# Performance work log

Measured on AMD Instinct MI355X. Metric: run time of the kernel, lower is better.

Reference implementation:

```python
import jax, jax.numpy as jnp
import numpy as np

N = 100000
E = 800000
NODE_DIM = 128
EDGE_DIM = 8
NUM_HEADS = 8
HEAD_DIM = NODE_DIM // NUM_HEADS


def setup_inputs() -> dict:
    key = jax.random.key(0)
    k_x, k_ei, k_ea, k_w1, k_b1, k_w2, k_b2 = jax.random.split(key, 7)
    x = jax.random.normal(k_x, (N, NODE_DIM), dtype=jnp.float32)
    edge_index = jax.random.randint(k_ei, (2, E), 0, N, dtype=jnp.int32)
    edge_attr = jax.random.normal(k_ea, (E, EDGE_DIM), dtype=jnp.float32)
    # node_proj: Linear(node_dim, node_dim)
    lim1 = 1.0 / np.sqrt(NODE_DIM)
    W_node = jax.random.uniform(k_w1, (NODE_DIM, NODE_DIM), minval=-lim1, maxval=lim1, dtype=jnp.float32)
    b_node = jax.random.uniform(k_b1, (NODE_DIM,), minval=-lim1, maxval=lim1, dtype=jnp.float32)
    # edge_to_attn: Linear(edge_dim, num_heads) followed by sigmoid
    lim2 = 1.0 / np.sqrt(EDGE_DIM)
    W_edge = jax.random.uniform(k_w2, (NUM_HEADS, EDGE_DIM), minval=-lim2, maxval=lim2, dtype=jnp.float32)
    b_edge = jax.random.uniform(k_b2, (NUM_HEADS,), minval=-lim2, maxval=lim2, dtype=jnp.float32)
    return {"x": x, "edge_index": edge_index, "edge_attr": edge_attr,
            "W_node": W_node, "b_node": b_node, "W_edge": W_edge, "b_edge": b_edge}


def reference(x, edge_index, edge_attr, W_node, b_node, W_edge, b_edge):
    # project node features: [N, node_dim]
    x_proj = x @ W_node.T + b_node
    # per-edge, per-head sigmoid gates: [E, H]
    edge_gates = jax.nn.sigmoid(edge_attr @ W_edge.T + b_edge)
    source = edge_index[0]
    target = edge_index[1]
    # gather source node features: [E, H, head_dim]
    x_source = x_proj[source].reshape(E, NUM_HEADS, HEAD_DIM)
    # gate and flatten messages: [E, node_dim]
    messages = (x_source * edge_gates[:, :, None]).reshape(E, NODE_DIM)
    # scatter-add to target nodes: [N, node_dim]
    out = jax.ops.segment_sum(messages, target, num_segments=N)
    return out
```

## Files before the change

kernel.cpp:

```cpp
#include <hip/hip_runtime.h>

typedef unsigned short u16;
typedef unsigned int u32;
typedef __attribute__((ext_vector_type(8))) short short8;
typedef __attribute__((ext_vector_type(4))) float f32x4;

constexpr int NODES = 100000;
constexpr int EDGES = 800000;
constexpr int DIM = 128;
constexpr int EDIM = 8;
constexpr int HEADS = 8;

__device__ inline u16 f2bf(float f) {
    u32 u = __float_as_uint(f);
    u = (u + 0x7FFFu + ((u >> 16) & 1u)) >> 16;
    return (u16)u;
}
__device__ inline float bf2f(u16 s) {
    return __uint_as_float(((u32)s) << 16);
}
__device__ inline u32 packbf(float a, float b) {
    return (u32)f2bf(a) | ((u32)f2bf(b) << 16);
}

__global__ __launch_bounds__(256) void convert_w(const float* __restrict__ W,
                                                 u16* __restrict__ Wb) {
    int i = blockIdx.x * 256 + threadIdx.x;
    Wb[i] = f2bf(W[i]);
}

__global__ __launch_bounds__(256) void node_proj_mfma(const float* __restrict__ x,
                                                      const u16* __restrict__ Wb,
                                                      const float* __restrict__ bn,
                                                      u16* __restrict__ xpb) {
    __shared__ u16 sW[128 * 136];

    const int tid = threadIdx.x;
    {
        const short8* g = reinterpret_cast<const short8*>(Wb);
        #pragma unroll
        for (int i = tid; i < 128 * 16; i += 256) {
            int row = i >> 4, ch = i & 15;
            *reinterpret_cast<short8*>(&sW[row * 136 + ch * 8]) = g[row * 16 + ch];
        }
    }
    __syncthreads();

    const int w = tid >> 6;
    const int l = tid & 63;
    const int lr = l & 15;
    const int lh = l >> 4;
    const int m0 = blockIdx.x * 128 + w * 32;

    f32x4 acc[2][8];
    #pragma unroll
    for (int mt = 0; mt < 2; ++mt)
        #pragma unroll
        for (int nt = 0; nt < 8; ++nt) acc[mt][nt] = f32x4{0, 0, 0, 0};

    #pragma unroll
    for (int kk = 0; kk < 4; ++kk) {
        const int kb = kk * 32 + lh * 8;
        short8 a0, a1;
        {
            int row = m0 + lr;  row = row < NODES ? row : 0;
            const float* p = x + (size_t)row * DIM + kb;
            float4 f0 = *reinterpret_cast<const float4*>(p);
            float4 f1 = *reinterpret_cast<const float4*>(p + 4);
            a0[0]=f2bf(f0.x); a0[1]=f2bf(f0.y); a0[2]=f2bf(f0.z); a0[3]=f2bf(f0.w);
            a0[4]=f2bf(f1.x); a0[5]=f2bf(f1.y); a0[6]=f2bf(f1.z); a0[7]=f2bf(f1.w);
        }
        {
            int row = m0 + 16 + lr;  row = row < NODES ? row : 0;
            const float* p = x + (size_t)row * DIM + kb;
            float4 f0 = *reinterpret_cast<const float4*>(p);
            float4 f1 = *reinterpret_cast<const float4*>(p + 4);
            a1[0]=f2bf(f0.x); a1[1]=f2bf(f0.y); a1[2]=f2bf(f0.z); a1[3]=f2bf(f0.w);
            a1[4]=f2bf(f1.x); a1[5]=f2bf(f1.y); a1[6]=f2bf(f1.z); a1[7]=f2bf(f1.w);
        }
        #pragma unroll
        for (int nt = 0; nt < 8; ++nt) {
            short8 b = *reinterpret_cast<const short8*>(&sW[(nt * 16 + lr) * 136 + kb]);
            acc[0][nt] = __builtin_amdgcn_mfma_f32_16x16x32_bf16(a0, b, acc[0][nt], 0, 0, 0);
            acc[1][nt] = __builtin_amdgcn_mfma_f32_16x16x32_bf16(a1, b, acc[1][nt], 0, 0, 0);
        }
    }

    float bias[8];
    #pragma unroll
    for (int nt = 0; nt < 8; ++nt) bias[nt] = bn[nt * 16 + lr];

    #pragma unroll
    for (int mt = 0; mt < 2; ++mt) {
        #pragma unroll
        for (int r = 0; r < 4; ++r) {
            int grow = m0 + mt * 16 + lh * 4 + r;
            if (grow < NODES) {
                #pragma unroll
                for (int nt = 0; nt < 8; ++nt)
                    xpb[(size_t)grow * DIM + nt * 16 + lr] =
                        f2bf(acc[mt][nt][r] + bias[nt]);
            }
        }
    }
}

__global__ __launch_bounds__(256) void build_rec(const int* __restrict__ ei,
                                                 const float* __restrict__ ea,
                                                 const float* __restrict__ We,
                                                 const float* __restrict__ be,
                                                 int* __restrict__ head,
                                                 uint4* __restrict__ rec) {
    __shared__ float sW[HEADS * EDIM];
    __shared__ float sb[HEADS];
    if (threadIdx.x < HEADS * EDIM) sW[threadIdx.x] = We[threadIdx.x];
    if (threadIdx.x < HEADS) sb[threadIdx.x] = be[threadIdx.x];
    __syncthreads();

    const int e = blockIdx.x * 256 + threadIdx.x;
    if (e >= EDGES) return;

    const int src = ei[e];
    const int tgt = ei[EDGES + e];
    float4 a0 = *reinterpret_cast<const float4*>(ea + (size_t)e * EDIM);
    float4 a1 = *reinterpret_cast<const float4*>(ea + (size_t)e * EDIM + 4);

    float g[HEADS];
    #pragma unroll
    for (int h = 0; h < HEADS; ++h) {
        const float* w = &sW[h * EDIM];
        float z = sb[h]
                + a0.x * w[0] + a0.y * w[1] + a0.z * w[2] + a0.w * w[3]
                + a1.x * w[4] + a1.y * w[5] + a1.z * w[6] + a1.w * w[7];
        g[h] = 1.0f / (1.0f + __expf(-z));
    }

    int nx = atomicExch(&head[tgt], e);

    uint4 r0, r1;
    r0.x = (u32)nx;
    r0.y = (u32)src;
    r0.z = packbf(g[0], g[1]);
    r0.w = packbf(g[2], g[3]);
    r1.x = packbf(g[4], g[5]);
    r1.y = packbf(g[6], g[7]);
    r1.z = 0; r1.w = 0;
    rec[(size_t)e * 2 + 0] = r0;
    rec[(size_t)e * 2 + 1] = r1;
}

__global__ __launch_bounds__(256) void aggregate_v6(const u16* __restrict__ xpb,
                                                    const int* __restrict__ head,
                                                    const char* __restrict__ recB,
                                                    float* __restrict__ out) {
    const int n = blockIdx.x * 16 + (threadIdx.x >> 4);
    if (n >= NODES) return;
    const int l = threadIdx.x & 15;
    const int h = l >> 1;

    float acc[8];
    #pragma unroll
    for (int i = 0; i < 8; ++i) acc[i] = 0.0f;

    int e = head[n];
    while (e >= 0) {
        const char* r = recB + (size_t)e * 32;
        int2 ns = *reinterpret_cast<const int2*>(r);
        float g = bf2f(*reinterpret_cast<const u16*>(r + 8 + 2 * h));
        short8 u = *reinterpret_cast<const short8*>(
            xpb + (size_t)ns.y * DIM + l * 8);
        #pragma unroll
        for (int i = 0; i < 8; ++i) acc[i] += g * bf2f((u16)u[i]);
        e = ns.x;
    }

    float4 o0 = {acc[0], acc[1], acc[2], acc[3]};
    float4 o1 = {acc[4], acc[5], acc[6], acc[7]};
    float4* op = reinterpret_cast<float4*>(out + (size_t)n * DIM + l * 8);
    op[0] = o0;
    op[1] = o1;
}

__global__ __launch_bounds__(256) void edge_scatter(const int* __restrict__ ei,
                                                    const float* __restrict__ ea,
                                                    const float* __restrict__ We,
                                                    const float* __restrict__ be,
                                                    const u16* __restrict__ xpb,
                                                    float* __restrict__ out) {
    __shared__ float sW[HEADS * EDIM];
    __shared__ float sb[HEADS];
    if (threadIdx.x < HEADS * EDIM) sW[threadIdx.x] = We[threadIdx.x];
    if (threadIdx.x < HEADS) sb[threadIdx.x] = be[threadIdx.x];
    __syncthreads();

    const int t = blockIdx.x * 256 + threadIdx.x;
    const int e = t >> 5;
    const int l = t & 31;
    if (e >= EDGES) return;

    const int src = ei[e];
    const int tgt = ei[EDGES + e];
    const int h = l >> 2;

    float4 ea0 = *reinterpret_cast<const float4*>(ea + (size_t)e * EDIM);
    float4 ea1 = *reinterpret_cast<const float4*>(ea + (size_t)e * EDIM + 4);
    float4 wa = *reinterpret_cast<const float4*>(&sW[h * EDIM]);
    float4 wb = *reinterpret_cast<const float4*>(&sW[h * EDIM + 4]);
    float z = sb[h]
            + ea0.x * wa.x + ea0.y * wa.y + ea0.z * wa.z + ea0.w * wa.w
            + ea1.x * wb.x + ea1.y * wb.y + ea1.z * wb.z + ea1.w * wb.w;
    float g = 1.0f / (1.0f + __expf(-z));

    ushort4 u = *reinterpret_cast<const ushort4*>(xpb + (size_t)src * DIM + l * 4);
    float* op = out + (size_t)tgt * DIM + l * 4;
    unsafeAtomicAdd(op + 0, bf2f(u.x) * g);
    unsafeAtomicAdd(op + 1, bf2f(u.y) * g);
    unsafeAtomicAdd(op + 2, bf2f(u.z) * g);
    unsafeAtomicAdd(op + 3, bf2f(u.w) * g);
}

extern "C" void kernel_launch(void* const* d_in, const int* in_sizes, int n_in,
                              void* d_out, int out_size, void* d_ws, size_t ws_size,
                              hipStream_t stream) {
    const float* x   = (const float*)d_in[0];
    const int*   ei  = (const int*)d_in[1];
    const float* eat = (const float*)d_in[2];
    const float* Wn  = (const float*)d_in[3];
    const float* bn  = (const float*)d_in[4];
    const float* We  = (const float*)d_in[5];
    const float* be  = (const float*)d_in[6];
    float* out = (float*)d_out;

    u16* Wb   = (u16*)d_ws;
    u16* xpb  = Wb + DIM * DIM;
    int* head = (int*)(xpb + (size_t)NODES * DIM);
    char* rec = (char*)(head + NODES);

    const size_t need = (size_t)(DIM * DIM) * 2 + (size_t)NODES * DIM * 2
                      + (size_t)NODES * 4 + (size_t)EDGES * 32;

    convert_w<<<64, 256, 0, stream>>>(Wn, Wb);
    node_proj_mfma<<<(NODES + 127) / 128, 256, 0, stream>>>(x, Wb, bn, xpb);

    if (ws_size >= need) {
        hipMemsetAsync(head, 0xFF, (size_t)NODES * sizeof(int), stream);
        build_rec<<<(EDGES + 255) / 256, 256, 0, stream>>>(ei, eat, We, be,
                                                           head, (uint4*)rec);
        aggregate_v6<<<(NODES + 15) / 16, 256, 0, stream>>>(xpb, head, rec, out);
    } else {
        hipMemsetAsync(d_out, 0, (size_t)out_size * sizeof(float), stream);
        edge_scatter<<<(EDGES * 32) / 256, 256, 0, stream>>>(ei, eat, We, be, xpb, out);
    }
}
```

Before: 121.2 us.

## Fuse projection and edge-record kernels; split adjacency lists into four interleaved chains

Merges weight conversion, node projection and edge-record building into one launch, with blocks split by index range, so the two independent stages can run concurrently and two launches disappear. Each node's linked list becomes four chains selected by edge index mod 4. The aggregation kernel then walks four chains at once, giving more independent memory loads in flight per step. In exchange, each projection block converts the weights to bf16 itself, the head array is four times larger, and lanes do masked extra work when chain lengths differ.

```diff
diff --git a/kernel.cpp b/kernel.cpp
--- a/kernel.cpp
+++ b/kernel.cpp
@@ -11,6 +11,9 @@
 constexpr int EDIM = 8;
 constexpr int HEADS = 8;
 
+constexpr int PROJ_BLOCKS = (NODES + 127) / 128;
+constexpr int REC_BLOCKS  = (EDGES + 255) / 256;
+
 __device__ inline u16 f2bf(float f) {
     u32 u = __float_as_uint(f);
     u = (u + 0x7FFFu + ((u >> 16) & 1u)) >> 16;
@@ -23,134 +26,141 @@
     return (u32)f2bf(a) | ((u32)f2bf(b) << 16);
 }
 
-__global__ __launch_bounds__(256) void convert_w(const float* __restrict__ W,
-                                                 u16* __restrict__ Wb) {
-    int i = blockIdx.x * 256 + threadIdx.x;
-    Wb[i] = f2bf(W[i]);
-}
-
-__global__ __launch_bounds__(256) void node_proj_mfma(const float* __restrict__ x,
-                                                      const u16* __restrict__ Wb,
-                                                      const float* __restrict__ bn,
-                                                      u16* __restrict__ xpb) {
-    __shared__ u16 sW[128 * 136];
+__global__ __launch_bounds__(256) void prep_fused(const float* __restrict__ x,
+                                                  const float* __restrict__ Wn,
+                                                  const float* __restrict__ bn,
+                                                  const int* __restrict__ ei,
+                                                  const float* __restrict__ ea,
+                                                  const float* __restrict__ We,
+                                                  const float* __restrict__ be,
+                                                  int* __restrict__ head4,
+                                                  uint4* __restrict__ rec,
+                                                  u16* __restrict__ xpb) {
+    __shared__ u16 sLds[128 * 136];
 
     const int tid = threadIdx.x;
-    {
-        const short8* g = reinterpret_cast<const short8*>(Wb);
-        #pragma unroll
-        for (int i = tid; i < 128 * 16; i += 256) {
-            int row = i >> 4, ch = i & 15;
-            *reinterpret_cast<short8*>(&sW[row * 136 + ch * 8]) = g[row * 16 + ch];
-        }
+
+    if (blockIdx.x < PROJ_BLOCKS) {
+        {
+            #pragma unroll
+            for (int i = tid; i < 128 * 16; i += 256) {
+                int row = i >> 4, ch = i & 15;
+                const float* p = Wn + row * DIM + ch * 8;
+                float4 f0 = *reinterpret_cast<const float4*>(p);
+                float4 f1 = *reinterpret_cast<const float4*>(p + 4);
+                short8 v;
+                v[0]=(short)f2bf(f0.x); v[1]=(short)f2bf(f0.y);
+                v[2]=(short)f2bf(f0.z); v[3]=(short)f2bf(f0.w);
+                v[4]=(short)f2bf(f1.x); v[5]=(short)f2bf(f1.y);
+                v[6]=(short)f2bf(f1.z); v[7]=(short)f2bf(f1.w);
+                *reinterpret_cast<short8*>(&sLds[row * 136 + ch * 8]) = v;
+            }
+        }
+        __syncthreads();
+
+        const int w = tid >> 6;
+        const int l = tid & 63;
+        const int lr = l & 15;
+        const int lh = l >> 4;
+        const int m0 = blockIdx.x * 128 + w * 32;
+
+        f32x4 acc[2][8];
+        #pragma unroll
+        for (int mt = 0; mt < 2; ++mt)
+            #pragma unroll
+            for (int nt = 0; nt < 8; ++nt) acc[mt][nt] = f32x4{0, 0, 0, 0};
+
+        #pragma unroll
+        for (int kk = 0; kk < 4; ++kk) {
+            const int kb = kk * 32 + lh * 8;
+            short8 a0, a1;
+            {
+                int row = m0 + lr;  row = row < NODES ? row : 0;
+                const float* p = x + (size_t)row * DIM + kb;
+                float4 f0 = *reinterpret_cast<const float4*>(p);
+                float4 f1 = *reinterpret_cast<const float4*>(p + 4);
+                a0[0]=(short)f2bf(f0.x); a0[1]=(short)f2bf(f0.y);
+                a0[2]=(short)f2bf(f0.z); a0[3]=(short)f2bf(f0.w);
+                a0[4]=(short)f2bf(f1.x); a0[5]=(short)f2bf(f1.y);
+                a0[6]=(short)f2bf(f1.z); a0[7]=(short)f2bf(f1.w);
+            }
+            {
+                int row = m0 + 16 + lr;  row = row < NODES ? row : 0;
+                const float* p = x + (size_t)row * DIM + kb;
+                float4 f0 = *reinterpret_cast<const float4*>(p);
+                float4 f1 = *reinterpret_cast<const float4*>(p + 4);
+                a1[0]=(short)f2bf(f0.x); a1[1]=(short)f2bf(f0.y);
+                a1[2]=(short)f2bf(f0.z); a1[3]=(short)f2bf(f0.w);
+                a1[4]=(short)f2bf(f1.x); a1[5]=(short)f2bf(f1.y);
+                a1[6]=(short)f2bf(f1.z); a1[7]=(short)f2bf(f1.w);
+            }
+            #pragma unroll
+            for (int nt = 0; nt < 8; ++nt) {
+                short8 b = *reinterpret_cast<const short8*>(&sLds[(nt * 16 + lr) * 136 + kb]);
+                acc[0][nt] = __builtin_amdgcn_mfma_f32_16x16x32_bf16(a0, b, acc[0][nt], 0, 0, 0);
+                acc[1][nt] = __builtin_amdgcn_mfma_f32_16x16x32_bf16(a1, b, acc[1][nt], 0, 0, 0);
+            }
+        }
+
+        float bias[8];
+        #pragma unroll
+        for (int nt = 0; nt < 8; ++nt) bias[nt] = bn[nt * 16 + lr];
+
+        #pragma unroll
+        for (int mt = 0; mt < 2; ++mt) {
+            #pragma unroll
+            for (int r = 0; r < 4; ++r) {
+                int grow = m0 + mt * 16 + lh * 4 + r;
+                if (grow < NODES) {
+                    #pragma unroll
+                    for (int nt = 0; nt < 8; ++nt)
+                        xpb[(size_t)grow * DIM + nt * 16 + lr] =
+                            f2bf(acc[mt][nt][r] + bias[nt]);
+                }
+            }
+        }
+    } else {
+        float* sW = reinterpret_cast<float*>(sLds);
+        float* sb = sW + HEADS * EDIM;
+        if (tid < HEADS * EDIM) sW[tid] = We[tid];
+        if (tid < HEADS) sb[tid] = be[tid];
+        __syncthreads();
+
+        const int e = (blockIdx.x - PROJ_BLOCKS) * 256 + tid;
+        if (e >= EDGES) return;
+
+        const int src = ei[e];
+        const int tgt = ei[EDGES + e];
+        float4 a0 = *reinterpret_cast<const float4*>(ea + (size_t)e * EDIM);
+        float4 a1 = *reinterpret_cast<const float4*>(ea + (size_t)e * EDIM + 4);
+
+        float g[HEADS];
+        #pragma unroll
+        for (int h = 0; h < HEADS; ++h) {
+            const float* w = &sW[h * EDIM];
+            float z = sb[h]
+                    + a0.x * w[0] + a0.y * w[1] + a0.z * w[2] + a0.w * w[3]
+                    + a1.x * w[4] + a1.y * w[5] + a1.z * w[6] + a1.w * w[7];
+            g[h] = 1.0f / (1.0f + __expf(-z));
+        }
+
+        int nx = atomicExch(&head4[tgt * 4 + (e & 3)], e);
+
+        uint4 r0, r1;
+        r0.x = (u32)nx;
+        r0.y = (u32)src;
+        r0.z = packbf(g[0], g[1]);
+        r0.w = packbf(g[2], g[3]);
+        r1.x = packbf(g[4], g[5]);
+        r1.y = packbf(g[6], g[7]);
+        r1.z = 0; r1.w = 0;
+        rec[(size_t)e * 2 + 0] = r0;
+        rec[(size_t)e * 2 + 1] = r1;
     }
-    __syncthreads();
-
-    const int w = tid >> 6;
-    const int l = tid & 63;
-    const int lr = l & 15;
-    const int lh = l >> 4;
-    const int m0 = blockIdx.x * 128 + w * 32;
-
-    f32x4 acc[2][8];
-    #pragma unroll
-    for (int mt = 0; mt < 2; ++mt)
-        #pragma unroll
-        for (int nt = 0; nt < 8; ++nt) acc[mt][nt] = f32x4{0, 0, 0, 0};
-
-    #pragma unroll
-    for (int kk = 0; kk < 4; ++kk) {
-        const int kb = kk * 32 + lh * 8;
-        short8 a0, a1;
-        {
-            int row = m0 + lr;  row = row < NODES ? row : 0;
-            const float* p = x + (size_t)row * DIM + kb;
-            float4 f0 = *reinterpret_cast<const float4*>(p);
-            float4 f1 = *reinterpret_cast<const float4*>(p + 4);
-            a0[0]=f2bf(f0.x); a0[1]=f2bf(f0.y); a0[2]=f2bf(f0.z); a0[3]=f2bf(f0.w);
-            a0[4]=f2bf(f1.x); a0[5]=f2bf(f1.y); a0[6]=f2bf(f1.z); a0[7]=f2bf(f1.w);
-        }
-        {
-            int row = m0 + 16 + lr;  row = row < NODES ? row : 0;
-            const float* p = x + (size_t)row * DIM + kb;
-            float4 f0 = *reinterpret_cast<const float4*>(p);
-            float4 f1 = *reinterpret_cast<const float4*>(p + 4);
-            a1[0]=f2bf(f0.x); a1[1]=f2bf(f0.y); a1[2]=f2bf(f0.z); a1[3]=f2bf(f0.w);
-            a1[4]=f2bf(f1.x); a1[5]=f2bf(f1.y); a1[6]=f2bf(f1.z); a1[7]=f2bf(f1.w);
-        }
-        #pragma unroll
-        for (int nt = 0; nt < 8; ++nt) {
-            short8 b = *reinterpret_cast<const short8*>(&sW[(nt * 16 + lr) * 136 + kb]);
-            acc[0][nt] = __builtin_amdgcn_mfma_f32_16x16x32_bf16(a0, b, acc[0][nt], 0, 0, 0);
-            acc[1][nt] = __builtin_amdgcn_mfma_f32_16x16x32_bf16(a1, b, acc[1][nt], 0, 0, 0);
-        }
-    }
-
-    float bias[8];
-    #pragma unroll
-    for (int nt = 0; nt < 8; ++nt) bias[nt] = bn[nt * 16 + lr];
-
-    #pragma unroll
-    for (int mt = 0; mt < 2; ++mt) {
-        #pragma unroll
-        for (int r = 0; r < 4; ++r) {
-            int grow = m0 + mt * 16 + lh * 4 + r;
-            if (grow < NODES) {
-                #pragma unroll
-                for (int nt = 0; nt < 8; ++nt)
-                    xpb[(size_t)grow * DIM + nt * 16 + lr] =
-                        f2bf(acc[mt][nt][r] + bias[nt]);
-            }
-        }
-    }
-}
-
-__global__ __launch_bounds__(256) void build_rec(const int* __restrict__ ei,
-                                                 const float* __restrict__ ea,
-                                                 const float* __restrict__ We,
-                                                 const float* __restrict__ be,
-                                                 int* __restrict__ head,
-                                                 uint4* __restrict__ rec) {
-    __shared__ float sW[HEADS * EDIM];
-    __shared__ float sb[HEADS];
-    if (threadIdx.x < HEADS * EDIM) sW[threadIdx.x] = We[threadIdx.x];
-    if (threadIdx.x < HEADS) sb[threadIdx.x] = be[threadIdx.x];
-    __syncthreads();
-
-    const int e = blockIdx.x * 256 + threadIdx.x;
-    if (e >= EDGES) return;
-
-    const int src = ei[e];
-    const int tgt = ei[EDGES + e];
-    float4 a0 = *reinterpret_cast<const float4*>(ea + (size_t)e * EDIM);
-    float4 a1 = *reinterpret_cast<const float4*>(ea + (size_t)e * EDIM + 4);
-
-    float g[HEADS];
-    #pragma unroll
-    for (int h = 0; h < HEADS; ++h) {
-        const float* w = &sW[h * EDIM];
-        float z = sb[h]
-                + a0.x * w[0] + a0.y * w[1] + a0.z * w[2] + a0.w * w[3]
-                + a1.x * w[4] + a1.y * w[5] + a1.z * w[6] + a1.w * w[7];
-        g[h] = 1.0f / (1.0f + __expf(-z));
-    }
-
-    int nx = atomicExch(&head[tgt], e);
-
-    uint4 r0, r1;
-    r0.x = (u32)nx;
-    r0.y = (u32)src;
-    r0.z = packbf(g[0], g[1]);
-    r0.w = packbf(g[2], g[3]);
-    r1.x = packbf(g[4], g[5]);
-    r1.y = packbf(g[6], g[7]);
-    r1.z = 0; r1.w = 0;
-    rec[(size_t)e * 2 + 0] = r0;
-    rec[(size_t)e * 2 + 1] = r1;
-}
-
-__global__ __launch_bounds__(256) void aggregate_v6(const u16* __restrict__ xpb,
-                                                    const int* __restrict__ head,
+}
+
+__global__ __launch_bounds__(256) void aggregate_v7(const u16* __restrict__ xpb,
+                                                    const int* __restrict__ head4,
                                                     const char* __restrict__ recB,
                                                     float* __restrict__ out) {
     const int n = blockIdx.x * 16 + (threadIdx.x >> 4);
@@ -162,16 +172,47 @@
     #pragma unroll
     for (int i = 0; i < 8; ++i) acc[i] = 0.0f;
 
-    int e = head[n];
-    while (e >= 0) {
-        const char* r = recB + (size_t)e * 32;
-        int2 ns = *reinterpret_cast<const int2*>(r);
-        float g = bf2f(*reinterpret_cast<const u16*>(r + 8 + 2 * h));
-        short8 u = *reinterpret_cast<const short8*>(
-            xpb + (size_t)ns.y * DIM + l * 8);
-        #pragma unroll
-        for (int i = 0; i < 8; ++i) acc[i] += g * bf2f((u16)u[i]);
-        e = ns.x;
+    int e0 = head4[n * 4 + 0];
+    int e1 = head4[n * 4 + 1];
+    int e2 = head4[n * 4 + 2];
+    int e3 = head4[n * 4 + 3];
+
+    while (e0 >= 0 || e1 >= 0 || e2 >= 0 || e3 >= 0) {
+        int c0 = e0 >= 0 ? e0 : 0;
+        int c1 = e1 >= 0 ? e1 : 0;
+        int c2 = e2 >= 0 ? e2 : 0;
+        int c3 = e3 >= 0 ? e3 : 0;
+        const char* r0 = recB + (size_t)c0 * 32;
+        const char* r1 = recB + (size_t)c1 * 32;
+        const char* r2 = recB + (size_t)c2 * 32;
+        const char* r3 = recB + (size_t)c3 * 32;
+        int2 ns0 = *reinterpret_cast<const int2*>(r0);
+        int2 ns1 = *reinterpret_cast<const int2*>(r1);
+        int2 ns2 = *reinterpret_cast<const int2*>(r2);
+        int2 ns3 = *reinterpret_cast<const int2*>(r3);
+        float g0 = bf2f(*reinterpret_cast<const u16*>(r0 + 8 + 2 * h));
+        float g1 = bf2f(*reinterpret_cast<const u16*>(r1 + 8 + 2 * h));
+        float g2 = bf2f(*reinterpret_cast<const u16*>(r2 + 8 + 2 * h));
+        float g3 = bf2f(*reinterpret_cast<const u16*>(r3 + 8 + 2 * h));
+        short8 u0 = *reinterpret_cast<const short8*>(xpb + (size_t)ns0.y * DIM + l * 8);
+        short8 u1 = *reinterpret_cast<const short8*>(xpb + (size_t)ns1.y * DIM + l * 8);
+        short8 u2 = *reinterpret_cast<const short8*>(xpb + (size_t)ns2.y * DIM + l * 8);
+        short8 u3 = *reinterpret_cast<const short8*>(xpb + (size_t)ns3.y * DIM + l * 8);
+        float m0 = e0 >= 0 ? g0 : 0.0f;
+        float m1 = e1 >= 0 ? g1 : 0.0f;
+        float m2 = e2 >= 0 ? g2 : 0.0f;
+        float m3 = e3 >= 0 ? g3 : 0.0f;
+        #pragma unroll
+        for (int i = 0; i < 8; ++i) {
+            acc[i] += m0 * bf2f((u16)u0[i]);
+            acc[i] += m1 * bf2f((u16)u1[i]);
+            acc[i] += m2 * bf2f((u16)u2[i]);
+            acc[i] += m3 * bf2f((u16)u3[i]);
+        }
+        e0 = e0 >= 0 ? ns0.x : -1;
+        e1 = e1 >= 0 ? ns1.x : -1;
+        e2 = e2 >= 0 ? ns2.x : -1;
+        e3 = e3 >= 0 ? ns3.x : -1;
     }
 
     float4 o0 = {acc[0], acc[1], acc[2], acc[3]};
@@ -231,23 +272,22 @@
     const float* be  = (const float*)d_in[6];
     float* out = (float*)d_out;
 
-    u16* Wb   = (u16*)d_ws;
-    u16* xpb  = Wb + DIM * DIM;
-    int* head = (int*)(xpb + (size_t)NODES * DIM);
-    char* rec = (char*)(head + NODES);
-
-    const size_t need = (size_t)(DIM * DIM) * 2 + (size_t)NODES * DIM * 2
-                      + (size_t)NODES * 4 + (size_t)EDGES * 32;
-
-    convert_w<<<64, 256, 0, stream>>>(Wn, Wb);
-    node_proj_mfma<<<(NODES + 127) / 128, 256, 0, stream>>>(x, Wb, bn, xpb);
+    u16* xpb   = (u16*)d_ws;
+    int* head4 = (int*)(xpb + (size_t)NODES * DIM);
+    char* rec  = (char*)(head4 + (size_t)NODES * 4);
+
+    const size_t need = (size_t)NODES * DIM * 2 + (size_t)NODES * 16
+                      + (size_t)EDGES * 32;
+    const size_t need_fb = (size_t)NODES * DIM * 2;
 
     if (ws_size >= need) {
-        hipMemsetAsync(head, 0xFF, (size_t)NODES * sizeof(int), stream);
-        build_rec<<<(EDGES + 255) / 256, 256, 0, stream>>>(ei, eat, We, be,
-                                                           head, (uint4*)rec);
-        aggregate_v6<<<(NODES + 15) / 16, 256, 0, stream>>>(xpb, head, rec, out);
-    } else {
+        hipMemsetAsync(head4, 0xFF, (size_t)NODES * 16, stream);
+        prep_fused<<<PROJ_BLOCKS + REC_BLOCKS, 256, 0, stream>>>(
+            x, Wn, bn, ei, eat, We, be, head4, (uint4*)rec, xpb);
+        aggregate_v7<<<(NODES + 15) / 16, 256, 0, stream>>>(xpb, head4, rec, out);
+    } else if (ws_size >= need_fb) {
+        prep_fused<<<PROJ_BLOCKS, 256, 0, stream>>>(
+            x, Wn, bn, ei, eat, We, be, nullptr, nullptr, xpb);
         hipMemsetAsync(d_out, 0, (size_t)out_size * sizeof(float), stream);
         edge_scatter<<<(EDGES * 32) / 256, 256, 0, stream>>>(ei, eat, We, be, xpb, out);
     }
```

New measurement: 112.4 us. 7.3% less time.
